# Performance work log

Hardware: AMD Instinct MI355X
Metric: run time of the kernel (lower is better)

The kernel has to match this reference:

```python
import jax, jax.numpy as jnp
import numpy as np

D_MODEL = 1024
B, T = 4, 2048
LN_EPS = 1e-5


def setup_inputs() -> dict:
    key = jax.random.key(0)
    ks = jax.random.split(key, 8)
    d = D_MODEL
    x = jax.random.normal(ks[0], (B, T, d), dtype=jnp.float32)
    # linear params (fan-in scaled)
    W_in = jax.random.normal(ks[1], (d, 4 * d), dtype=jnp.float32) / np.sqrt(d)
    b_in = jnp.zeros((4 * d,), dtype=jnp.float32)
    W_out = jax.random.normal(ks[2], (2 * d, d), dtype=jnp.float32) / np.sqrt(2 * d)
    b_out = jnp.zeros((d,), dtype=jnp.float32)
    # LRU initializer (matches the torch module's initializer())
    rng = np.random.default_rng(0)
    r_min, r_max = 0.9, 0.999
    u1 = rng.random(d)
    u2 = rng.random(d)
    nu_log = np.log(-0.5 * np.log(u1 * (r_max ** 2 - r_min ** 2) + r_min ** 2))
    theta_log = np.log(u2 * np.pi * 2)
    gamma_log = np.log(np.sqrt(1 - np.exp(-np.exp(nu_log)) ** 2))
    # LayerNorm affine params
    ln_w = jnp.ones((2 * d,), dtype=jnp.float32)
    ln_b = jnp.zeros((2 * d,), dtype=jnp.float32)
    return {
        "x": x,
        "W_in": W_in, "b_in": b_in,
        "nu_log": jnp.asarray(nu_log, dtype=jnp.float32),
        "theta_log": jnp.asarray(theta_log, dtype=jnp.float32),
        "gamma_log": jnp.asarray(gamma_log, dtype=jnp.float32),
        "ln_w": ln_w, "ln_b": ln_b,
        "W_out": W_out, "b_out": b_out,
    }


def _complex_scan(in_r, in_i, f_r, f_i):
    """h_t = f * h_{t-1} + in_t over axis=1, complex math in real/imag pairs."""
    def combine(l, r):
        a1r, a1i, b1r, b1i = l
        a2r, a2i, b2r, b2i = r
        ar = a2r * a1r - a2i * a1i
        ai = a2r * a1i + a2i * a1r
        br = a2r * b1r - a2i * b1i + b2r
        bi = a2r * b1i + a2i * b1r + b2i
        return (ar, ai, br, bi)
    fr = jnp.broadcast_to(f_r, in_r.shape)
    fi = jnp.broadcast_to(f_i, in_i.shape)
    _, _, hr, hi = jax.lax.associative_scan(combine, (fr, fi, in_r, in_i), axis=1)
    return hr, hi


def reference(x, W_in, b_in, nu_log, theta_log, gamma_log, ln_w, ln_b, W_out, b_out):
    d = x.shape[-1]
    u = x @ W_in + b_in                       # [B, T, 4d]
    v, o = u[..., :2 * d], u[..., 2 * d:]     # each [B, T, 2d]
    nu = jnp.exp(-jnp.exp(nu_log))            # [d]
    theta = jnp.exp(theta_log)
    gamma = jnpp_exp = jnp.exp(gamma_log)
    f_r = nu * jnp.cos(theta)
    f_i = nu * jnp.sin(theta)
    in_r = gamma * v[..., :d]                 # [B, T, d]
    in_i = gamma * v[..., d:]
    h_r, h_i = _complex_scan(in_r, in_i, f_r, f_i)
    y = jnp.concatenate([h_r, h_i], axis=-1) * jax.nn.silu(o)  # [B, T, 2d]
    mu = jnp.mean(y, axis=-1, keepdims=True)
    var = jnp.mean(jnp.square(y - mu), axis=-1, keepdims=True)
    y = (y - mu) * jax.lax.rsqrt(var + LN_EPS) * ln_w + ln_b
    return y @ W_out + b_out                  # [B, T, d]
```

## Files before the change

### kernel.cpp

```cpp
#include <hip/hip_runtime.h>
#include <hip/hip_bf16.h>

#define D_MODEL 1024
#define BB 4
#define TT 2048
#define ROWS (BB*TT)
#define NCHUNK 32
#define CHLEN 64

typedef __attribute__((ext_vector_type(8))) short short8;
typedef __attribute__((ext_vector_type(4))) float floatx4;

static __device__ __forceinline__ ushort f2bf(float f) {
    union { float f; unsigned u; } v; v.f = f;
    unsigned r = v.u + 0x7FFF + ((v.u >> 16) & 1);
    return (ushort)(r >> 16);
}
static __device__ __forceinline__ float bf2f(ushort b) {
    union { unsigned u; float f; } v; v.u = ((unsigned)b) << 16;
    return v.f;
}

#define GLOAD_LDS16(gp, lp)                                                 \
    __builtin_amdgcn_global_load_lds(                                       \
        (const __attribute__((address_space(1))) void*)(gp),                \
        (__attribute__((address_space(3))) void*)(lp), 16, 0, 0)


__global__ __launch_bounds__(256) void cvt_x(const float* __restrict__ x,
                                             ushort* __restrict__ xb) {
    int i = blockIdx.x * 256 + threadIdx.x;
    float4 v = ((const float4*)x)[i];
    ushort4 o;
    o.x = f2bf(v.x); o.y = f2bf(v.y); o.z = f2bf(v.z); o.w = f2bf(v.w);
    ((ushort4*)xb)[i] = o;
}

__global__ __launch_bounds__(256) void transp_cvt(const float* __restrict__ W,
                                                  ushort* __restrict__ WT,
                                                  int K, int N) {
    __shared__ float tile[32][33];
    int n0 = blockIdx.x * 32, k0 = blockIdx.y * 32;
    int tx = threadIdx.x & 31, ty = threadIdx.x >> 5;
#pragma unroll
    for (int j = 0; j < 4; ++j)
        tile[ty + j*8][tx] = W[(size_t)(k0 + ty + j*8) * N + n0 + tx];
    __syncthreads();
#pragma unroll
    for (int j = 0; j < 4; ++j)
        WT[(size_t)(n0 + ty + j*8) * K + k0 + tx] = f2bf(tile[tx][ty + j*8]);
}

__global__ void consts_k(const float* __restrict__ nu_log,
                         const float* __restrict__ theta_log,
                         const float* __restrict__ gamma_log,
                         float* __restrict__ fr, float* __restrict__ fi,
                         float* __restrict__ gm) {
    int c = blockIdx.x * 256 + threadIdx.x;
    if (c < D_MODEL) {
        float nu = expf(-expf(nu_log[c]));
        float th = expf(theta_log[c]);
        fr[c] = nu * cosf(th);
        fi[c] = nu * sinf(th);
        gm[c] = expf(gamma_log[c]);
    }
}

__global__ __launch_bounds__(256) void gemm_bf16(
    const ushort* __restrict__ A, const ushort* __restrict__ B,
    int K, int N, const float* __restrict__ bias, int mode,
    const float* __restrict__ gamma,
    ushort* __restrict__ out_r, ushort* __restrict__ out_i,
    ushort* __restrict__ out_o, float* __restrict__ outC) {
    __shared__ ushort As[128 * 64];
    __shared__ ushort Bs[128 * 64];
    int tid = threadIdx.x;
    int lane = tid & 63, wave = tid >> 6;
    int wm = (wave & 1) * 64, wn = (wave >> 1) * 64;
    int lr = lane & 15, q = lane >> 4;
    long m0 = (long)blockIdx.y * 128;
    long n0 = (long)blockIdx.x * 128;
    floatx4 acc[4][4] = {};

    int rs = tid >> 3;
    int pg = ((tid & 7) ^ (rs & 7)) * 8;
    const ushort* Ap = A + (m0 + rs) * (long)K + pg;
    const ushort* Bp = B + (n0 + rs) * (long)K + pg;
    int swl = lr & 7;

    for (int kt = 0; kt < K; kt += 64) {
        __syncthreads();
#pragma unroll
        for (int j = 0; j < 4; ++j) {
            GLOAD_LDS16(Ap + kt + (long)(j * 32) * K, &As[(j * 256 + tid) * 8]);
            GLOAD_LDS16(Bp + kt + (long)(j * 32) * K, &Bs[(j * 256 + tid) * 8]);
        }
        __syncthreads();
#pragma unroll
        for (int s = 0; s < 2; ++s) {
            short8 af[4], bfv[4];
            int pq = ((s * 4 + q) ^ swl) * 8;
#pragma unroll
            for (int r = 0; r < 4; ++r)
                af[r] = *(const short8*)&As[(wm + r * 16 + lr) * 64 + pq];
#pragma unroll
            for (int c = 0; c < 4; ++c)
                bfv[c] = *(const short8*)&Bs[(wn + c * 16 + lr) * 64 + pq];
#pragma unroll
            for (int r = 0; r < 4; ++r)
#pragma unroll
                for (int c = 0; c < 4; ++c)
                    acc[r][c] = __builtin_amdgcn_mfma_f32_16x16x32_bf16(
                        af[r], bfv[c], acc[r][c], 0, 0, 0);
        }
    }

    if (mode == 0) {
#pragma unroll
        for (int r = 0; r < 4; ++r) {
#pragma unroll
            for (int c = 0; c < 4; ++c) {
                long col = n0 + wn + c * 16 + lr;
                float bv = bias[col];
#pragma unroll
                for (int g = 0; g < 4; ++g) {
                    long row = m0 + wm + r * 16 + q * 4 + g;
                    outC[row * (long)N + col] = acc[r][c][g] + bv;
                }
            }
        }
    } else {
        int sector = (int)((n0 + wn) >> 10);
        int lc0 = (int)((n0 + wn) & 1023);
        if (sector < 2) {
            ushort* dst = sector ? out_i : out_r;
#pragma unroll
            for (int r = 0; r < 4; ++r) {
#pragma unroll
                for (int c = 0; c < 4; ++c) {
                    int lc = lc0 + c * 16 + lr;
                    float bv = bias[(sector << 10) + lc];
                    float gv = gamma[lc];
#pragma unroll
                    for (int g = 0; g < 4; ++g) {
                        long row = m0 + wm + r * 16 + q * 4 + g;
                        dst[row * 1024 + lc] = f2bf(gv * (acc[r][c][g] + bv));
                    }
                }
            }
        } else {
            int oc0 = (int)(n0 + wn - 2048);
#pragma unroll
            for (int r = 0; r < 4; ++r) {
#pragma unroll
                for (int c = 0; c < 4; ++c) {
                    int oc = oc0 + c * 16 + lr;
                    float bv = bias[2048 + oc];
#pragma unroll
                    for (int g = 0; g < 4; ++g) {
                        long row = m0 + wm + r * 16 + q * 4 + g;
                        out_o[row * 2048 + oc] = f2bf(acc[r][c][g] + bv);
                    }
                }
            }
        }
    }
}

__global__ __launch_bounds__(256) void scan_carries(
    const ushort* __restrict__ in_r, const ushort* __restrict__ in_i,
    float* __restrict__ carry,
    const float* __restrict__ fr_, const float* __restrict__ fi_) {
    int t = blockIdx.x * 256 + threadIdx.x;
    int c = t & 1023;
    int ck = (t >> 10) & (NCHUNK - 1);
    int b = t >> 15;
    float fr = fr_[c], fi = fi_[c];
    size_t base = ((size_t)(b * TT + ck * CHLEN)) * 1024 + c;
    float hr = 0.f, hi = 0.f;
#pragma unroll 4
    for (int j = 0; j < CHLEN; ++j) {
        size_t idx = base + (size_t)j * 1024;
        float r = bf2f(in_r[idx]), im = bf2f(in_i[idx]);
        float nhr = fr * hr - fi * hi + r;
        float nhi = fr * hi + fi * hr + im;
        hr = nhr; hi = nhi;
    }
    size_t ci = (((size_t)b * 1024 + c) * NCHUNK + ck) * 2;
    carry[ci] = hr; carry[ci + 1] = hi;
}

__global__ __launch_bounds__(256) void scan_apply(
    ushort* __restrict__ h_r, ushort* __restrict__ h_i,
    const float* __restrict__ carry,
    const float* __restrict__ fr_, const float* __restrict__ fi_) {
    int t = blockIdx.x * 256 + threadIdx.x;
    int c = t & 1023;
    int ck = (t >> 10) & (NCHUNK - 1);
    int b = t >> 15;
    float fr = fr_[c], fi = fi_[c];
    float ar = fr, ai = fi;
#pragma unroll
    for (int s = 0; s < 6; ++s) {
        float nr = ar * ar - ai * ai, ni = 2.f * ar * ai;
        ar = nr; ai = ni;
    }
    float Hr = 0.f, Hi = 0.f;
    size_t cb = ((size_t)b * 1024 + c) * NCHUNK * 2;
    for (int k = 0; k < ck; ++k) {
        float cr = carry[cb + k * 2], cim = carry[cb + k * 2 + 1];
        float nHr = ar * Hr - ai * Hi + cr;
        float nHi = ar * Hi + ai * Hr + cim;
        Hr = nHr; Hi = nHi;
    }
    size_t base = ((size_t)(b * TT + ck * CHLEN)) * 1024 + c;
    float hr = Hr, hi = Hi;
#pragma unroll 4
    for (int j = 0; j < CHLEN; ++j) {
        size_t idx = base + (size_t)j * 1024;
        float r = bf2f(h_r[idx]), im = bf2f(h_i[idx]);
        float nhr = fr * hr - fi * hi + r;
        float nhi = fr * hi + fi * hr + im;
        hr = nhr; hi = nhi;
        h_r[idx] = f2bf(hr); h_i[idx] = f2bf(hi);
    }
}

__global__ __launch_bounds__(256) void ln_fuse(
    const ushort* __restrict__ hr, const ushort* __restrict__ hi,
    const ushort* __restrict__ o, const float* __restrict__ lnw,
    const float* __restrict__ lnb, ushort* __restrict__ yb) {
    long row = blockIdx.x;
    int tid = threadIdx.x;
    float y[8];
    float s = 0.f, s2 = 0.f;
#pragma unroll
    for (int j = 0; j < 8; ++j) {
        int c = tid + j * 256;
        float ov = bf2f(o[row * 2048 + c]);
        float sg = 1.f / (1.f + __expf(-ov));
        float h = (j < 4) ? bf2f(hr[row * 1024 + c]) : bf2f(hi[row * 1024 + c - 1024]);
        float v = h * ov * sg;
        y[j] = v; s += v; s2 += v * v;
    }
#pragma unroll
    for (int off = 32; off > 0; off >>= 1) {
        s += __shfl_down(s, off, 64);
        s2 += __shfl_down(s2, off, 64);
    }
    __shared__ float red[8];
    int wv = tid >> 6;
    if ((tid & 63) == 0) { red[wv] = s; red[4 + wv] = s2; }
    __syncthreads();
    if (tid == 0) {
        red[0] = red[0] + red[1] + red[2] + red[3];
        red[4] = red[4] + red[5] + red[6] + red[7];
    }
    __syncthreads();
    s = red[0]; s2 = red[4];
    float mu = s * (1.f / 2048.f);
    float var = s2 * (1.f / 2048.f) - mu * mu;
    float rs = rsqrtf(var + 1e-5f);
#pragma unroll
    for (int j = 0; j < 8; ++j) {
        int c = tid + j * 256;
        float v = (y[j] - mu) * rs * lnw[c] + lnb[c];
        yb[row * 2048 + c] = f2bf(v);
    }
}


extern "C" void kernel_launch(void* const* d_in, const int* in_sizes, int n_in,
                              void* d_out, int out_size, void* d_ws, size_t ws_size,
                              hipStream_t stream) {
    const float* x         = (const float*)d_in[0];
    const float* W_in      = (const float*)d_in[1];
    const float* b_in      = (const float*)d_in[2];
    const float* nu_log    = (const float*)d_in[3];
    const float* theta_log = (const float*)d_in[4];
    const float* gamma_log = (const float*)d_in[5];
    const float* ln_w      = (const float*)d_in[6];
    const float* ln_b      = (const float*)d_in[7];
    const float* W_out     = (const float*)d_in[8];
    const float* b_out     = (const float*)d_in[9];
    float* out = (float*)d_out;

    char* ws = (char*)d_ws;
    size_t off = 0;
    auto alloc = [&](size_t bytes) {
        char* p = ws + off;
        off += (bytes + 255) & ~(size_t)255;
        return p;
    };
    ushort* xb    = (ushort*)alloc((size_t)ROWS * 1024 * 2);
    ushort* WinT  = (ushort*)alloc((size_t)4096 * 1024 * 2);
    ushort* WoutT = (ushort*)alloc((size_t)1024 * 2048 * 2);
    float*  fr    = (float*)alloc(1024 * 4);
    float*  fi    = (float*)alloc(1024 * 4);
    float*  gm    = (float*)alloc(1024 * 4);
    ushort* in_r  = (ushort*)alloc((size_t)ROWS * 1024 * 2);
    ushort* in_i  = (ushort*)alloc((size_t)ROWS * 1024 * 2);
    ushort* obuf  = (ushort*)alloc((size_t)ROWS * 2048 * 2);
    float*  carry = (float*)alloc((size_t)BB * 1024 * NCHUNK * 2 * 4);
    ushort* yb    = (ushort*)alloc((size_t)ROWS * 2048 * 2);

    cvt_x<<<ROWS * 1024 / 4 / 256, 256, 0, stream>>>(x, xb);
    transp_cvt<<<dim3(4096 / 32, 1024 / 32), 256, 0, stream>>>(W_in, WinT, 1024, 4096);
    transp_cvt<<<dim3(1024 / 32, 2048 / 32), 256, 0, stream>>>(W_out, WoutT, 2048, 1024);
    consts_k<<<4, 256, 0, stream>>>(nu_log, theta_log, gamma_log, fr, fi, gm);

    gemm_bf16<<<dim3(4096 / 128, ROWS / 128), 256, 0, stream>>>(
        xb, WinT, 1024, 4096, b_in, 1, gm, in_r, in_i, obuf, nullptr);

    scan_carries<<<BB * 1024 * NCHUNK / 256, 256, 0, stream>>>(in_r, in_i, carry, fr, fi);
    scan_apply<<<BB * 1024 * NCHUNK / 256, 256, 0, stream>>>(in_r, in_i, carry, fr, fi);

    ln_fuse<<<ROWS, 256, 0, stream>>>(in_r, in_i, obuf, ln_w, ln_b, yb);

    gemm_bf16<<<dim3(1024 / 128, ROWS / 128), 256, 0, stream>>>(
        yb, WoutT, 2048, 1024, b_out, 0, nullptr, nullptr, nullptr, nullptr, out);
}
```

Before: 307.5 us.

## Fold LayerNorm into output GEMM epilogue and fuse gating into scan

Merges the input-conversion and weight-transpose prep kernels into one launch, and folds ln_w into the transposed W_out. It also precomputes per-column sums (s1, c2) so LayerNorm becomes a per-row correction in the second GEMM's epilogue. scan_apply now computes h*silu(o) directly into yb instead of writing h back, and a lightweight row_stats kernel only computes mean and rstd. This removes one full read/write pass of the 2d activation and several launches. The trade-off is un-normalized bf16 values feeding the GEMM, with cancellation in acc - mu*s1, plus atomics in prep.

Result: faster. 296.8 us (-3.5%).

```diff
diff --git a/kernel.cpp b/kernel.cpp
--- a/kernel.cpp
+++ b/kernel.cpp
@@ -26,43 +26,76 @@
         (const __attribute__((address_space(1))) void*)(gp),                \
         (__attribute__((address_space(3))) void*)(lp), 16, 0, 0)
 
-
-__global__ __launch_bounds__(256) void cvt_x(const float* __restrict__ x,
-                                             ushort* __restrict__ xb) {
-    int i = blockIdx.x * 256 + threadIdx.x;
-    float4 v = ((const float4*)x)[i];
-    ushort4 o;
-    o.x = f2bf(v.x); o.y = f2bf(v.y); o.z = f2bf(v.z); o.w = f2bf(v.w);
-    ((ushort4*)xb)[i] = o;
-}
-
-__global__ __launch_bounds__(256) void transp_cvt(const float* __restrict__ W,
-                                                  ushort* __restrict__ WT,
-                                                  int K, int N) {
-    __shared__ float tile[32][33];
-    int n0 = blockIdx.x * 32, k0 = blockIdx.y * 32;
-    int tx = threadIdx.x & 31, ty = threadIdx.x >> 5;
-#pragma unroll
-    for (int j = 0; j < 4; ++j)
-        tile[ty + j*8][tx] = W[(size_t)(k0 + ty + j*8) * N + n0 + tx];
-    __syncthreads();
-#pragma unroll
-    for (int j = 0; j < 4; ++j)
-        WT[(size_t)(n0 + ty + j*8) * K + k0 + tx] = f2bf(tile[tx][ty + j*8]);
-}
-
-__global__ void consts_k(const float* __restrict__ nu_log,
-                         const float* __restrict__ theta_log,
-                         const float* __restrict__ gamma_log,
-                         float* __restrict__ fr, float* __restrict__ fi,
-                         float* __restrict__ gm) {
-    int c = blockIdx.x * 256 + threadIdx.x;
-    if (c < D_MODEL) {
-        float nu = expf(-expf(nu_log[c]));
-        float th = expf(theta_log[c]);
-        fr[c] = nu * cosf(th);
-        fi[c] = nu * sinf(th);
-        gm[c] = expf(gamma_log[c]);
+#define PREP_A 8192
+#define PREP_B 4096
+#define PREP_C 2048
+__global__ __launch_bounds__(256) void prep_all(
+    const float* __restrict__ x, ushort* __restrict__ xb,
+    const float* __restrict__ W_in, ushort* __restrict__ WinT,
+    const float* __restrict__ W_out, ushort* __restrict__ W1T,
+    const float* __restrict__ lnw, const float* __restrict__ lnb,
+    float* __restrict__ s1, float* __restrict__ c2,
+    const float* __restrict__ nu_log, const float* __restrict__ theta_log,
+    const float* __restrict__ gamma_log,
+    float* __restrict__ fr, float* __restrict__ fi, float* __restrict__ gm) {
+    __shared__ float smem[32 * 33 + 8 * 32 * 2];
+    int bid = blockIdx.x, tid = threadIdx.x;
+    if (bid < PREP_A) {
+        int i = bid * 256 + tid;
+        float4 v = ((const float4*)x)[i];
+        ushort4 o;
+        o.x = f2bf(v.x); o.y = f2bf(v.y); o.z = f2bf(v.z); o.w = f2bf(v.w);
+        ((ushort4*)xb)[i] = o;
+    } else if (bid < PREP_A + PREP_B) {
+        int b2 = bid - PREP_A;
+        int n0 = (b2 & 127) * 32, k0 = (b2 >> 7) * 32;
+        int tx = tid & 31, ty = tid >> 5;
+        float (*tile)[33] = (float (*)[33])smem;
+#pragma unroll
+        for (int j = 0; j < 4; ++j)
+            tile[ty + j*8][tx] = W_in[(size_t)(k0 + ty + j*8) * 4096 + n0 + tx];
+        __syncthreads();
+#pragma unroll
+        for (int j = 0; j < 4; ++j)
+            WinT[(size_t)(n0 + ty + j*8) * 1024 + k0 + tx] = f2bf(tile[tx][ty + j*8]);
+    } else if (bid < PREP_A + PREP_B + PREP_C) {
+        int b2 = bid - PREP_A - PREP_B;
+        int n0 = (b2 & 31) * 32, k0 = (b2 >> 5) * 32;
+        int tx = tid & 31, ty = tid >> 5;
+        float (*tile)[33] = (float (*)[33])smem;
+        float* red1 = smem + 32 * 33;
+        float* red2 = red1 + 8 * 32;
+        float p1 = 0.f, p2 = 0.f;
+#pragma unroll
+        for (int j = 0; j < 4; ++j) {
+            int k = k0 + ty + j * 8;
+            float w = W_out[(size_t)k * 1024 + n0 + tx];
+            float lw = lnw[k], lb = lnb[k];
+            tile[ty + j*8][tx] = lw * w;
+            p1 += lw * w; p2 += lb * w;
+        }
+        __syncthreads();
+#pragma unroll
+        for (int j = 0; j < 4; ++j)
+            W1T[(size_t)(n0 + ty + j*8) * 2048 + k0 + tx] = f2bf(tile[tx][ty + j*8]);
+        red1[ty * 32 + tx] = p1; red2[ty * 32 + tx] = p2;
+        __syncthreads();
+        if (ty == 0) {
+            float a = 0.f, b = 0.f;
+#pragma unroll
+            for (int t = 0; t < 8; ++t) { a += red1[t * 32 + tx]; b += red2[t * 32 + tx]; }
+            atomicAdd(&s1[n0 + tx], a);
+            atomicAdd(&c2[n0 + tx], b);
+        }
+    } else {
+        int c = (bid - PREP_A - PREP_B - PREP_C) * 256 + tid;
+        if (c < D_MODEL) {
+            float nu = expf(-expf(nu_log[c]));
+            float th = expf(theta_log[c]);
+            fr[c] = nu * cosf(th);
+            fi[c] = nu * sinf(th);
+            gm[c] = expf(gamma_log[c]);
+        }
     }
 }
 
@@ -71,7 +104,9 @@
     int K, int N, const float* __restrict__ bias, int mode,
     const float* __restrict__ gamma,
     ushort* __restrict__ out_r, ushort* __restrict__ out_i,
-    ushort* __restrict__ out_o, float* __restrict__ outC) {
+    ushort* __restrict__ out_o, float* __restrict__ outC,
+    const float* __restrict__ mu, const float* __restrict__ rs,
+    const float* __restrict__ s1, const float* __restrict__ c2) {
     __shared__ ushort As[128 * 64];
     __shared__ ushort Bs[128 * 64];
     int tid = threadIdx.x;
@@ -82,10 +117,10 @@
     long n0 = (long)blockIdx.x * 128;
     floatx4 acc[4][4] = {};
 
-    int rs = tid >> 3;
-    int pg = ((tid & 7) ^ (rs & 7)) * 8;
-    const ushort* Ap = A + (m0 + rs) * (long)K + pg;
-    const ushort* Bp = B + (n0 + rs) * (long)K + pg;
+    int rs_ = tid >> 3;
+    int pg = ((tid & 7) ^ (rs_ & 7)) * 8;
+    const ushort* Ap = A + (m0 + rs_) * (long)K + pg;
+    const ushort* Bp = B + (n0 + rs_) * (long)K + pg;
     int swl = lr & 7;
 
     for (int kt = 0; kt < K; kt += 64) {
@@ -115,17 +150,19 @@
         }
     }
 
-    if (mode == 0) {
+    if (mode == 2) {
 #pragma unroll
         for (int r = 0; r < 4; ++r) {
 #pragma unroll
             for (int c = 0; c < 4; ++c) {
                 long col = n0 + wn + c * 16 + lr;
-                float bv = bias[col];
+                float bc = c2[col] + bias[col];
+                float s1c = s1[col];
 #pragma unroll
                 for (int g = 0; g < 4; ++g) {
                     long row = m0 + wm + r * 16 + q * 4 + g;
-                    outC[row * (long)N + col] = acc[r][c][g] + bv;
+                    outC[row * (long)N + col] =
+                        rs[row] * (acc[r][c][g] - mu[row] * s1c) + bc;
                 }
             }
         }
@@ -191,9 +228,10 @@
 }
 
 __global__ __launch_bounds__(256) void scan_apply(
-    ushort* __restrict__ h_r, ushort* __restrict__ h_i,
+    const ushort* __restrict__ in_r, const ushort* __restrict__ in_i,
     const float* __restrict__ carry,
-    const float* __restrict__ fr_, const float* __restrict__ fi_) {
+    const float* __restrict__ fr_, const float* __restrict__ fi_,
+    const ushort* __restrict__ o, ushort* __restrict__ yb) {
     int t = blockIdx.x * 256 + threadIdx.x;
     int c = t & 1023;
     int ck = (t >> 10) & (NCHUNK - 1);
@@ -214,34 +252,39 @@
         Hr = nHr; Hi = nHi;
     }
     size_t base = ((size_t)(b * TT + ck * CHLEN)) * 1024 + c;
+    size_t rowbase = (size_t)(b * TT + ck * CHLEN);
     float hr = Hr, hi = Hi;
-#pragma unroll 4
+#pragma unroll 2
     for (int j = 0; j < CHLEN; ++j) {
         size_t idx = base + (size_t)j * 1024;
-        float r = bf2f(h_r[idx]), im = bf2f(h_i[idx]);
+        float r = bf2f(in_r[idx]), im = bf2f(in_i[idx]);
         float nhr = fr * hr - fi * hi + r;
         float nhi = fr * hi + fi * hr + im;
         hr = nhr; hi = nhi;
-        h_r[idx] = f2bf(hr); h_i[idx] = f2bf(hi);
-    }
-}
-
-__global__ __launch_bounds__(256) void ln_fuse(
-    const ushort* __restrict__ hr, const ushort* __restrict__ hi,
-    const ushort* __restrict__ o, const float* __restrict__ lnw,
-    const float* __restrict__ lnb, ushort* __restrict__ yb) {
+        size_t ob = (rowbase + j) * 2048 + c;
+        float ov1 = bf2f(o[ob]);
+        float ov2 = bf2f(o[ob + 1024]);
+        float y1 = hr * ov1 / (1.f + __expf(-ov1));
+        float y2 = hi * ov2 / (1.f + __expf(-ov2));
+        yb[ob] = f2bf(y1);
+        yb[ob + 1024] = f2bf(y2);
+    }
+}
+
+__global__ __launch_bounds__(256) void row_stats(
+    const ushort* __restrict__ yb, float* __restrict__ mu_o,
+    float* __restrict__ rs_o) {
     long row = blockIdx.x;
     int tid = threadIdx.x;
-    float y[8];
+    const ushort* p = yb + row * 2048 + tid * 8;
+    uint4 raw = *(const uint4*)p;
     float s = 0.f, s2 = 0.f;
-#pragma unroll
-    for (int j = 0; j < 8; ++j) {
-        int c = tid + j * 256;
-        float ov = bf2f(o[row * 2048 + c]);
-        float sg = 1.f / (1.f + __expf(-ov));
-        float h = (j < 4) ? bf2f(hr[row * 1024 + c]) : bf2f(hi[row * 1024 + c - 1024]);
-        float v = h * ov * sg;
-        y[j] = v; s += v; s2 += v * v;
+    unsigned w[4] = {raw.x, raw.y, raw.z, raw.w};
+#pragma unroll
+    for (int j = 0; j < 4; ++j) {
+        float a = bf2f((ushort)(w[j] & 0xffff));
+        float b = bf2f((ushort)(w[j] >> 16));
+        s += a + b; s2 += a * a + b * b;
     }
 #pragma unroll
     for (int off = 32; off > 0; off >>= 1) {
@@ -253,19 +296,12 @@
     if ((tid & 63) == 0) { red[wv] = s; red[4 + wv] = s2; }
     __syncthreads();
     if (tid == 0) {
-        red[0] = red[0] + red[1] + red[2] + red[3];
-        red[4] = red[4] + red[5] + red[6] + red[7];
-    }
-    __syncthreads();
-    s = red[0]; s2 = red[4];
-    float mu = s * (1.f / 2048.f);
-    float var = s2 * (1.f / 2048.f) - mu * mu;
-    float rs = rsqrtf(var + 1e-5f);
-#pragma unroll
-    for (int j = 0; j < 8; ++j) {
-        int c = tid + j * 256;
-        float v = (y[j] - mu) * rs * lnw[c] + lnb[c];
-        yb[row * 2048 + c] = f2bf(v);
+        s = red[0] + red[1] + red[2] + red[3];
+        s2 = red[4] + red[5] + red[6] + red[7];
+        float mu = s * (1.f / 2048.f);
+        float var = s2 * (1.f / 2048.f) - mu * mu;
+        mu_o[row] = mu;
+        rs_o[row] = rsqrtf(var + 1e-5f);
     }
 }
 
@@ -294,29 +330,38 @@
     };
     ushort* xb    = (ushort*)alloc((size_t)ROWS * 1024 * 2);
     ushort* WinT  = (ushort*)alloc((size_t)4096 * 1024 * 2);
-    ushort* WoutT = (ushort*)alloc((size_t)1024 * 2048 * 2);
+    ushort* W1T   = (ushort*)alloc((size_t)1024 * 2048 * 2);
     float*  fr    = (float*)alloc(1024 * 4);
     float*  fi    = (float*)alloc(1024 * 4);
     float*  gm    = (float*)alloc(1024 * 4);
+    float*  s1c2  = (float*)alloc(2048 * 4);
+    float*  s1    = s1c2;
+    float*  c2    = s1c2 + 1024;
     ushort* in_r  = (ushort*)alloc((size_t)ROWS * 1024 * 2);
     ushort* in_i  = (ushort*)alloc((size_t)ROWS * 1024 * 2);
     ushort* obuf  = (ushort*)alloc((size_t)ROWS * 2048 * 2);
     float*  carry = (float*)alloc((size_t)BB * 1024 * NCHUNK * 2 * 4);
     ushort* yb    = (ushort*)alloc((size_t)ROWS * 2048 * 2);
-
-    cvt_x<<<ROWS * 1024 / 4 / 256, 256, 0, stream>>>(x, xb);
-    transp_cvt<<<dim3(4096 / 32, 1024 / 32), 256, 0, stream>>>(W_in, WinT, 1024, 4096);
-    transp_cvt<<<dim3(1024 / 32, 2048 / 32), 256, 0, stream>>>(W_out, WoutT, 2048, 1024);
-    consts_k<<<4, 256, 0, stream>>>(nu_log, theta_log, gamma_log, fr, fi, gm);
+    float*  muv   = (float*)alloc(ROWS * 4);
+    float*  rsv   = (float*)alloc(ROWS * 4);
+
+    hipMemsetAsync(s1c2, 0, 2048 * 4, stream);
+
+    prep_all<<<PREP_A + PREP_B + PREP_C + 4, 256, 0, stream>>>(
+        x, xb, W_in, WinT, W_out, W1T, ln_w, ln_b, s1, c2,
+        nu_log, theta_log, gamma_log, fr, fi, gm);
 
     gemm_bf16<<<dim3(4096 / 128, ROWS / 128), 256, 0, stream>>>(
-        xb, WinT, 1024, 4096, b_in, 1, gm, in_r, in_i, obuf, nullptr);
+        xb, WinT, 1024, 4096, b_in, 1, gm, in_r, in_i, obuf, nullptr,
+        nullptr, nullptr, nullptr, nullptr);
 
     scan_carries<<<BB * 1024 * NCHUNK / 256, 256, 0, stream>>>(in_r, in_i, carry, fr, fi);
-    scan_apply<<<BB * 1024 * NCHUNK / 256, 256, 0, stream>>>(in_r, in_i, carry, fr, fi);
-
-    ln_fuse<<<ROWS, 256, 0, stream>>>(in_r, in_i, obuf, ln_w, ln_b, yb);
+    scan_apply<<<BB * 1024 * NCHUNK / 256, 256, 0, stream>>>(
+        in_r, in_i, carry, fr, fi, obuf, yb);
+
+    row_stats<<<ROWS, 256, 0, stream>>>(yb, muv, rsv);
 
     gemm_bf16<<<dim3(1024 / 128, ROWS / 128), 256, 0, stream>>>(
-        yb, WoutT, 2048, 1024, b_out, 0, nullptr, nullptr, nullptr, nullptr, out);
-}
+        yb, W1T, 2048, 1024, b_out, 2, nullptr, nullptr, nullptr, nullptr, out,
+        muv, rsv, s1, c2);
+}
```
